# Kernel optimization log

Measured on AMD Instinct MI355X. Metric: run time of the kernel, lower is better.

## Reference

```python
import jax, jax.numpy as jnp
import numpy as np
import math

D = 1024
H = 16
FF = 4096
BS = 4
N = 1024
NEG_INF = -jnp.inf


def layer_norm(x, g, b, eps=1e-5):
    mu = jnp.mean(x, axis=-1, keepdims=True)
    var = jnp.var(x, axis=-1, keepdims=True)
    return (x - mu) * jax.lax.rsqrt(var + eps) * g + b


def mha(x, kv, Wq, Wk, Wv, g, b, causal):
    bs, n, d = x.shape
    n_kv = kv.shape[1]
    hd = d // H
    q = (x @ Wq).reshape(bs, n, H, hd)
    k = (kv @ Wk).reshape(bs, n_kv, H, hd)
    v = (kv @ Wv).reshape(bs, n_kv, H, hd)
    # scores scaled by 1/sqrt(model_dim) as in the original (not head_dim!)
    scores = jnp.einsum('bihd,bjhd->bhij', q, k) / math.sqrt(d)
    if causal:
        i = jnp.arange(n)[:, None]
        j = jnp.arange(n_kv)[None, :]
        scores = jnp.where(j <= i, scores, NEG_INF)
    probs = jax.nn.softmax(scores, axis=-1)
    ctx = jnp.einsum('bhij,bjhd->bihd', probs, v).reshape(bs, n, d)
    return layer_norm(ctx + x, g, b)


def setup_inputs() -> dict:
    key = jax.random.key(0)
    ks = jax.random.split(key, 20)
    s_attn = 1.0 / math.sqrt(D)
    s_ff1 = 1.0 / math.sqrt(D)
    s_ff2 = 1.0 / math.sqrt(FF)
    return {
        'x': jax.random.normal(ks[0], (BS, N, D), jnp.float32),
        'encoder_out': jax.random.normal(ks[1], (BS, N, D), jnp.float32),
        'Wq1': jax.random.normal(ks[2], (D, D), jnp.float32) * s_attn,
        'Wk1': jax.random.normal(ks[3], (D, D), jnp.float32) * s_attn,
        'Wv1': jax.random.normal(ks[4], (D, D), jnp.float32) * s_attn,
        'g1': jnp.ones((D,), jnp.float32), 'b1': jnp.zeros((D,), jnp.float32),
        'Wq2': jax.random.normal(ks[5], (D, D), jnp.float32) * s_attn,
        'Wk2': jax.random.normal(ks[6], (D, D), jnp.float32) * s_attn,
        'Wv2': jax.random.normal(ks[7], (D, D), jnp.float32) * s_attn,
        'g2': jnp.ones((D,), jnp.float32), 'b2': jnp.zeros((D,), jnp.float32),
        'W_ff1': jax.random.normal(ks[8], (D, FF), jnp.float32) * s_ff1,
        'b_ff1': jnp.zeros((FF,), jnp.float32),
        'W_ff2': jax.random.normal(ks[9], (FF, D), jnp.float32) * s_ff2,
        'b_ff2': jnp.zeros((D,), jnp.float32),
        'g3': jnp.ones((D,), jnp.float32), 'b3': jnp.zeros((D,), jnp.float32),
    }


def reference(x, encoder_out, Wq1, Wk1, Wv1, g1, b1, Wq2, Wk2, Wv2, g2, b2,
              W_ff1, b_ff1, W_ff2, b_ff2, g3, b3):
    # masked (causal) self-attention
    x = mha(x, x, Wq1, Wk1, Wv1, g1, b1, causal=True)
    # cross-attention over encoder output
    x = mha(x, encoder_out, Wq2, Wk2, Wv2, g2, b2, causal=False)
    # feedforward with exact GELU, residual, layernorm
    h = jax.nn.gelu(x @ W_ff1 + b_ff1, approximate=False)
    out = h @ W_ff2 + b_ff2
    return layer_norm(out + x, g3, b3)
```

## Files before the change

kernel.cpp:

```cpp
#include <hip/hip_runtime.h>

typedef unsigned short u16;
typedef short bf16x8 __attribute__((ext_vector_type(8)));
typedef float f32x4 __attribute__((ext_vector_type(4)));
typedef unsigned short u16x8 __attribute__((ext_vector_type(8)));
typedef unsigned short u16x4 __attribute__((ext_vector_type(4)));

__device__ __forceinline__ u16 f2bf(float f) {
  unsigned u = __builtin_bit_cast(unsigned, f);
  u += 0x7fffu + ((u >> 16) & 1u);
  return (u16)(u >> 16);
}
__device__ __forceinline__ float bf2f(u16 v) {
  return __builtin_bit_cast(float, (unsigned)v << 16);
}

__device__ __forceinline__ void gload_lds16(const void* g, void* l) {
  __builtin_amdgcn_global_load_lds(
      (const __attribute__((address_space(1))) unsigned int*)g,
      (__attribute__((address_space(3))) unsigned int*)l, 16, 0, 0);
}

__global__ __launch_bounds__(256) void cast2_bf16_kernel(const float* __restrict__ s0,
                                                         u16* __restrict__ d0,
                                                         const float* __restrict__ s1,
                                                         u16* __restrict__ d1) {
  const float* s = blockIdx.y ? s1 : s0;
  u16* d = blockIdx.y ? d1 : d0;
  const size_t i = (size_t)blockIdx.x * 256 + threadIdx.x;
  const float4 a = ((const float4*)s)[2 * i];
  const float4 b = ((const float4*)s)[2 * i + 1];
  u16x8 o;
  o[0] = f2bf(a.x); o[1] = f2bf(a.y); o[2] = f2bf(a.z); o[3] = f2bf(a.w);
  o[4] = f2bf(b.x); o[5] = f2bf(b.y); o[6] = f2bf(b.z); o[7] = f2bf(b.w);
  ((u16x8*)d)[i] = o;
}

__global__ __launch_bounds__(256) void pack_bt3_kernel(const float* __restrict__ W0,
                                                       const float* __restrict__ W1,
                                                       const float* __restrict__ W2,
                                                       u16* __restrict__ Bt,
                                                       int K, int N) {
  const float* W = blockIdx.z == 0 ? W0 : (blockIdx.z == 1 ? W1 : W2);
  u16* dst0 = Bt + (size_t)blockIdx.z * K * N;
  __shared__ u16 sh[64][72];
  const int n0 = blockIdx.x * 64, k0 = blockIdx.y * 64;
  const int t = threadIdx.x;
  {
    const int kloc = t >> 2, nc = (t & 3) * 16;
    const float* src = W + (size_t)(k0 + kloc) * N + n0 + nc;
#pragma unroll
    for (int i = 0; i < 16; ++i) sh[kloc][nc + i] = f2bf(src[i]);
  }
  __syncthreads();
  {
    const int nloc = t >> 2, kc = (t & 3) * 16;
    u16 tmp[16];
#pragma unroll
    for (int i = 0; i < 16; ++i) tmp[i] = sh[kc + i][nloc];
    u16* dst = dst0 + (size_t)(n0 + nloc) * K + k0 + kc;
    *(u16x8*)dst = *(const u16x8*)tmp;
    *(u16x8*)(dst + 8) = *(const u16x8*)(tmp + 8);
  }
}

__global__ __launch_bounds__(256) void pack_bt_kernel(const float* __restrict__ W,
                                                      u16* __restrict__ Bt,
                                                      int K, int N) {
  __shared__ u16 sh[64][72];
  const int n0 = blockIdx.x * 64, k0 = blockIdx.y * 64;
  const int t = threadIdx.x;
  {
    const int kloc = t >> 2, nc = (t & 3) * 16;
    const float* src = W + (size_t)(k0 + kloc) * N + n0 + nc;
#pragma unroll
    for (int i = 0; i < 16; ++i) sh[kloc][nc + i] = f2bf(src[i]);
  }
  __syncthreads();
  {
    const int nloc = t >> 2, kc = (t & 3) * 16;
    u16 tmp[16];
#pragma unroll
    for (int i = 0; i < 16; ++i) tmp[i] = sh[kc + i][nloc];
    u16* dst = Bt + (size_t)(n0 + nloc) * K + k0 + kc;
    *(u16x8*)dst = *(const u16x8*)tmp;
    *(u16x8*)(dst + 8) = *(const u16x8*)(tmp + 8);
  }
}

template <int EPI, int VOUT>
__global__ __launch_bounds__(512, 4) void gemm_bt(const u16* __restrict__ A,
                                                  const u16* __restrict__ Bt,
                                                  void* __restrict__ Cout,
                                                  const float* __restrict__ bias,
                                                  u16* __restrict__ vt, int voff,
                                                  int M, int N, int K, int lda, int ldb) {
  __shared__ u16 lds[2][2][128 * 64];
  const int tid = threadIdx.x;
  const int lane = tid & 63;
  const int wid = tid >> 6;
  const int wr = wid >> 2;
  const int wc = wid & 3;
  const int g = lane >> 4, cc = lane & 15;
  const int nb = N >> 7;
  const int nwg = gridDim.x;
  const int cpx = nwg >> 3;
  const int bid = (blockIdx.x & 7) * cpx + (blockIdx.x >> 3);
  const int bm = bid / nb, bn = bid % nb;
  const size_t arow0 = (size_t)bm << 7;
  const size_t brow0 = (size_t)bn << 7;
  const size_t koff = (size_t)blockIdx.y * K;

  const u16* ap[2];
  const u16* bp[2];
  int ldst[2];
#pragma unroll
  for (int i = 0; i < 2; ++i) {
    const int tt = i * 512 + tid;
    const int row = tt >> 3;
    const int sc8 = ((tt & 7) ^ (row & 7)) * 8;
    ap[i] = A + (arow0 + row) * lda + koff + sc8;
    bp[i] = Bt + (brow0 + row) * ldb + koff + sc8;
    ldst[i] = (i * 512 + wid * 64) * 8;
  }

  int aoff[4], boff[2];
#pragma unroll
  for (int m = 0; m < 4; ++m) {
    const int rowa = wr * 64 + m * 16 + cc;
    aoff[m] = rowa * 128 + ((g ^ (rowa & 7)) << 4);
  }
#pragma unroll
  for (int n = 0; n < 2; ++n) {
    const int rowb = wc * 32 + n * 16 + cc;
    boff[n] = rowb * 128 + ((g ^ (rowb & 7)) << 4);
  }

  f32x4 acc[4][2] = {};
  const int nk = K >> 6;

#pragma unroll
  for (int i = 0; i < 2; ++i) {
    gload_lds16(ap[i], &lds[0][0][ldst[i]]);
    gload_lds16(bp[i], &lds[0][1][ldst[i]]);
    ap[i] += 64;
    bp[i] += 64;
  }
  __syncthreads();

  int cur = 0;
  for (int kk = 0; kk < nk; ++kk) {
    if (kk + 1 < nk) {
#pragma unroll
      for (int i = 0; i < 2; ++i) {
        gload_lds16(ap[i], &lds[cur ^ 1][0][ldst[i]]);
        gload_lds16(bp[i], &lds[cur ^ 1][1][ldst[i]]);
        ap[i] += 64;
        bp[i] += 64;
      }
    }
    const char* Al = (const char*)&lds[cur][0][0];
    const char* Bl = (const char*)&lds[cur][1][0];
    __builtin_amdgcn_s_setprio(1);
#pragma unroll
    for (int ks = 0; ks < 2; ++ks) {
      const int xr = ks << 6;
      bf16x8 af[4], bfr[2];
#pragma unroll
      for (int m = 0; m < 4; ++m)
        af[m] = *(const bf16x8*)(Al + (aoff[m] ^ xr));
#pragma unroll
      for (int n = 0; n < 2; ++n)
        bfr[n] = *(const bf16x8*)(Bl + (boff[n] ^ xr));
#pragma unroll
      for (int m = 0; m < 4; ++m)
#pragma unroll
        for (int n = 0; n < 2; ++n)
          acc[m][n] = __builtin_amdgcn_mfma_f32_16x16x32_bf16(af[m], bfr[n],
                                                              acc[m][n], 0, 0, 0);
    }
    __builtin_amdgcn_s_setprio(0);
    __syncthreads();
    cur ^= 1;
  }

  const size_t pout = (size_t)blockIdx.y * M * N;
#pragma unroll
  for (int m = 0; m < 4; ++m) {
    const size_t gr0 = arow0 + wr * 64 + m * 16 + (g << 2);
#pragma unroll
    for (int n = 0; n < 2; ++n) {
      const size_t gc = brow0 + wc * 32 + n * 16 + cc;
      if (VOUT && (int)gc >= voff) {
        const int col = (int)gc - voff;
        const int hh = col >> 6, dd = col & 63;
        const int bb = (int)(gr0 >> 10), nn = (int)(gr0 & 1023);
        u16x4 ov;
#pragma unroll
        for (int r = 0; r < 4; ++r) ov[r] = f2bf(acc[m][n][r]);
        *(u16x4*)&vt[(((size_t)(bb * 16 + hh) * 64 + dd) << 10) + nn] = ov;
        continue;
      }
      float bv = 0.f;
      if constexpr (EPI == 1) bv = bias[gc];
#pragma unroll
      for (int r = 0; r < 4; ++r) {
        float v = acc[m][n][r] + bv;
        const size_t idx = (gr0 + r) * (size_t)N + gc;
        if constexpr (EPI == 1) {
          const float u2 = 1.5957691216f * (v + 0.044715f * v * v * v);
          const float e = __expf(u2);
          v = v * e / (e + 1.f);
          ((u16*)Cout)[idx] = f2bf(v);
        } else if constexpr (EPI == 0) {
          ((u16*)Cout)[idx] = f2bf(v);
        } else {
          ((float*)Cout)[pout + idx] = v;
        }
      }
    }
  }
}

template <int CAUSAL>
__global__ __launch_bounds__(256, 6) void attn_kernel(const u16* __restrict__ Qb,
                                                      const u16* __restrict__ Kb,
                                                      const u16* __restrict__ Vt,
                                                      u16* __restrict__ Opart,
                                                      float* __restrict__ lpart,
                                                      int qstride, int kstride) {
  const int qt = blockIdx.x;
  const int bh = blockIdx.y;
  const int z = blockIdx.z;
  const int b = bh >> 4, h = bh & 15;
  const int lane = threadIdx.x & 63;
  const int w = threadIdx.x >> 6;
  const int g = lane >> 4, c = lane & 15;
  const int qbase = qt * 64 + w * 16;

  u16* Op = Opart + (size_t)z * 4096 * 1024;
  float* lp = lpart + (size_t)z * 64 * 1024 + (size_t)bh * 1024;

  int kt0 = z * 8, kt1 = z * 8 + 8;
  if (CAUSAL) kt1 = min(kt1, qt + 1);

  if (kt1 <= kt0) {
#pragma unroll
    for (int r = 0; r < 4; ++r) {
      const int qrow = qbase + g * 4 + r;
      u16x4 zz = {0, 0, 0, 0};
      *(u16x4*)&Op[(size_t)(b * 1024 + qrow) * 1024 + h * 64 + c * 4] = zz;
      if (c == 0) lp[qrow] = 0.f;
    }
    return;
  }

  bf16x8 qf0, qf1;
  {
    const int qrow = qbase + c;
    const u16* qp = Qb + (size_t)(b * 1024 + qrow) * qstride + h * 64 + g * 8;
    qf0 = *(const bf16x8*)qp;
    qf1 = *(const bf16x8*)(qp + 32);
  }

  float l_part[4] = {0.f, 0.f, 0.f, 0.f};
  f32x4 oacc[4] = {};

  __shared__ u16 Kl[64 * 64];
  __shared__ u16 Vl[64 * 64];
  __shared__ u16 Pl[4][16 * 72];
  u16* pw = &Pl[w][0];
  const int tid = threadIdx.x;

  for (int kt = kt0; kt < kt1; ++kt) {
    const int kv0 = kt * 64;
    __syncthreads();
#pragma unroll
    for (int i = 0; i < 2; ++i) {
      const int tt = i * 256 + tid;
      const int row = tt >> 3;
      const int sc = (tt & 7) ^ (row & 7);
      gload_lds16(Kb + (size_t)(b * 1024 + kv0 + row) * kstride + h * 64 + sc * 8,
                  &Kl[(size_t)(i * 256 + w * 64) * 8]);
      gload_lds16(Vt + ((size_t)bh * 64 + row) * 1024 + kv0 + sc * 8,
                  &Vl[(size_t)(i * 256 + w * 64) * 8]);
    }
    __syncthreads();

    f32x4 sacc[4] = {};
#pragma unroll
    for (int t = 0; t < 4; ++t) {
      const int row = t * 16 + c;
      const bf16x8 kf0 = *(const bf16x8*)&Kl[row * 64 + (g ^ (row & 7)) * 8];
      const bf16x8 kf1 = *(const bf16x8*)&Kl[row * 64 + ((4 + g) ^ (row & 7)) * 8];
      sacc[t] = __builtin_amdgcn_mfma_f32_16x16x32_bf16(qf0, kf0, sacc[t], 0, 0, 0);
      sacc[t] = __builtin_amdgcn_mfma_f32_16x16x32_bf16(qf1, kf1, sacc[t], 0, 0, 0);
    }
    const int qr0 = qbase + g * 4;
#pragma unroll
    for (int t = 0; t < 4; ++t) {
      const int kvcol = kv0 + t * 16 + c;
      const int col = t * 16 + c;
#pragma unroll
      for (int r = 0; r < 4; ++r) {
        float p = __expf(sacc[t][r] * 0.03125f);
        if (CAUSAL && kvcol > qr0 + r) p = 0.f;
        l_part[r] += p;
        pw[(g * 4 + r) * 72 + col] = f2bf(p);
      }
    }
#pragma unroll
    for (int ks = 0; ks < 2; ++ks) {
      const bf16x8 pa = *(const bf16x8*)&pw[c * 72 + ks * 32 + g * 8];
#pragma unroll
      for (int t2 = 0; t2 < 4; ++t2) {
        const int row = t2 * 16 + c;
        const bf16x8 vb =
            *(const bf16x8*)&Vl[row * 64 + ((ks * 4 + g) ^ (row & 7)) * 8];
        oacc[t2] = __builtin_amdgcn_mfma_f32_16x16x32_bf16(pa, vb, oacc[t2], 0, 0, 0);
      }
    }
  }
#pragma unroll
  for (int xm = 1; xm < 16; xm <<= 1)
#pragma unroll
    for (int r = 0; r < 4; ++r) l_part[r] += __shfl_xor(l_part[r], xm);
  if (c == 0) {
#pragma unroll
    for (int r = 0; r < 4; ++r) lp[qbase + g * 4 + r] = l_part[r];
  }
#pragma unroll
  for (int t2 = 0; t2 < 4; ++t2) {
    const int d = t2 * 16 + c;
#pragma unroll
    for (int r = 0; r < 4; ++r) {
      const int qrow = qbase + g * 4 + r;
      Op[(size_t)(b * 1024 + qrow) * 1024 + h * 64 + d] = f2bf(oacc[t2][r]);
    }
  }
}

template <int MODE, int RES_BF, int OUT_F>
__global__ __launch_bounds__(256) void add_ln_kernel(const void* __restrict__ a,
                                                     const float* __restrict__ lpart,
                                                     const void* __restrict__ res,
                                                     const float* __restrict__ gam,
                                                     const float* __restrict__ bet,
                                                     float* __restrict__ yf,
                                                     u16* __restrict__ ybf,
                                                     const float* __restrict__ bias) {
  const size_t row = blockIdx.x;
  const int t = threadIdx.x;
  float x[4];
  if constexpr (MODE == 1) {
    const u16* Ob = (const u16*)a;
    const u16x4 p0 = ((const u16x4*)(Ob + row * 1024))[t];
    const u16x4 p1 = ((const u16x4*)(Ob + (size_t)4096 * 1024 + row * 1024))[t];
    const int b = (int)(row >> 10), q = (int)(row & 1023);
    const int h = t >> 4;
    const size_t li = (size_t)(b * 16 + h) * 1024 + q;
    const float inv = 1.f / (lpart[li] + lpart[(size_t)64 * 1024 + li]);
#pragma unroll
    for (int i = 0; i < 4; ++i) x[i] = (bf2f(p0[i]) + bf2f(p1[i])) * inv;
  } else {
    const float* af = (const float*)a;
    float4 av = ((const float4*)(af + row * 1024))[t];
    const float4 a2 = ((const float4*)(af + (size_t)4096 * 1024 + row * 1024))[t];
    const float4 bv2 = ((const float4*)bias)[t];
    x[0] = av.x + a2.x + bv2.x; x[1] = av.y + a2.y + bv2.y;
    x[2] = av.z + a2.z + bv2.z; x[3] = av.w + a2.w + bv2.w;
  }
  if constexpr (RES_BF) {
    const u16x4 rv = ((const u16x4*)((const u16*)res + row * 1024))[t];
#pragma unroll
    for (int i = 0; i < 4; ++i) x[i] += bf2f(rv[i]);
  } else {
    const float4 rv = ((const float4*)((const float*)res + row * 1024))[t];
    x[0] += rv.x; x[1] += rv.y; x[2] += rv.z; x[3] += rv.w;
  }
  float s = x[0] + x[1] + x[2] + x[3];
  float q2 = x[0] * x[0] + x[1] * x[1] + x[2] * x[2] + x[3] * x[3];
#pragma unroll
  for (int m = 1; m < 64; m <<= 1) { s += __shfl_xor(s, m); q2 += __shfl_xor(q2, m); }
  __shared__ float ss[4], sq[4];
  const int w = t >> 6;
  if ((t & 63) == 0) { ss[w] = s; sq[w] = q2; }
  __syncthreads();
  s = ss[0] + ss[1] + ss[2] + ss[3];
  q2 = sq[0] + sq[1] + sq[2] + sq[3];
  const float mu = s * (1.f / 1024.f);
  const float var = q2 * (1.f / 1024.f) - mu * mu;
  const float rstd = rsqrtf(var + 1e-5f);
  const float4 gv = ((const float4*)gam)[t];
  const float4 bv = ((const float4*)bet)[t];
  float y[4];
  y[0] = (x[0] - mu) * rstd * gv.x + bv.x;
  y[1] = (x[1] - mu) * rstd * gv.y + bv.y;
  y[2] = (x[2] - mu) * rstd * gv.z + bv.z;
  y[3] = (x[3] - mu) * rstd * gv.w + bv.w;
  if constexpr (OUT_F) {
    float4 o; o.x = y[0]; o.y = y[1]; o.z = y[2]; o.w = y[3];
    ((float4*)(yf + row * 1024))[t] = o;
  } else {
    u16x4 ob;
    ob[0] = f2bf(y[0]); ob[1] = f2bf(y[1]); ob[2] = f2bf(y[2]); ob[3] = f2bf(y[3]);
    ((u16x4*)(ybf + row * 1024))[t] = ob;
  }
}

extern "C" void kernel_launch(void* const* d_in, const int* in_sizes, int n_in,
                              void* d_out, int out_size, void* d_ws, size_t ws_size,
                              hipStream_t stream) {
  const float* x    = (const float*)d_in[0];
  const float* enc  = (const float*)d_in[1];
  const float* Wq1  = (const float*)d_in[2];
  const float* Wk1  = (const float*)d_in[3];
  const float* Wv1  = (const float*)d_in[4];
  const float* g1   = (const float*)d_in[5];
  const float* b1   = (const float*)d_in[6];
  const float* Wq2  = (const float*)d_in[7];
  const float* Wk2  = (const float*)d_in[8];
  const float* Wv2  = (const float*)d_in[9];
  const float* g2   = (const float*)d_in[10];
  const float* b2   = (const float*)d_in[11];
  const float* Wff1 = (const float*)d_in[12];
  const float* bff1 = (const float*)d_in[13];
  const float* Wff2 = (const float*)d_in[14];
  const float* bff2 = (const float*)d_in[15];
  const float* g3   = (const float*)d_in[16];
  const float* b3   = (const float*)d_in[17];
  float* out = (float*)d_out;

  char* ws = (char*)d_ws;
  const size_t MB = 1024ull * 1024ull;
  u16*   bt  = (u16*)(ws + 0 * MB);
  u16*   big = (u16*)(ws + 8 * MB);
  u16*   vt  = (u16*)(ws + 40 * MB);
  float* ctx = (float*)(ws + 48 * MB);
  float* p1f = (float*)(ws + 64 * MB);
  u16*   abf = (u16*)(ws + 96 * MB);
  u16*   ebf = (u16*)(ws + 104 * MB);
  u16*   opart = (u16*)ctx;
  float* lpart = (float*)bt;
  (void)in_sizes; (void)n_in; (void)out_size; (void)ws_size;

  cast2_bf16_kernel<<<dim3(2048, 2), 256, 0, stream>>>(x, abf, enc, ebf);

  pack_bt3_kernel<<<dim3(16, 16, 3), 256, 0, stream>>>(Wq1, Wk1, Wv1, bt, 1024, 1024);
  gemm_bt<0, 1><<<(4096 / 128) * (3072 / 128), 512, 0, stream>>>(
      abf, bt, big, nullptr, vt, 2048, 4096, 3072, 1024, 1024, 1024);
  attn_kernel<1><<<dim3(16, 64, 2), 256, 0, stream>>>(big, big + 1024, vt, opart, lpart,
                                                      3072, 3072);
  add_ln_kernel<1, 0, 0><<<4096, 256, 0, stream>>>(opart, lpart, x, g1, b1,
                                                   nullptr, abf, nullptr);

  pack_bt3_kernel<<<dim3(16, 16, 3), 256, 0, stream>>>(Wq2, Wk2, Wv2, bt, 1024, 1024);
  u16* q2  = big;
  u16* kv2 = big + (size_t)4096 * 1024;
  gemm_bt<0, 0><<<(4096 / 128) * (1024 / 128), 512, 0, stream>>>(
      abf, bt, q2, nullptr, nullptr, 0, 4096, 1024, 1024, 1024, 1024);
  gemm_bt<0, 1><<<(4096 / 128) * (2048 / 128), 512, 0, stream>>>(
      ebf, bt + (size_t)1024 * 1024, kv2, nullptr, vt, 1024, 4096, 2048, 1024, 1024, 1024);
  attn_kernel<0><<<dim3(16, 64, 2), 256, 0, stream>>>(q2, kv2, vt, opart, lpart, 1024, 2048);
  add_ln_kernel<1, 1, 0><<<4096, 256, 0, stream>>>(opart, lpart, abf, g2, b2,
                                                   nullptr, abf, nullptr);

  pack_bt_kernel<<<dim3(64, 16), 256, 0, stream>>>(Wff1, bt, 1024, 4096);
  gemm_bt<1, 0><<<(4096 / 128) * (4096 / 128), 512, 0, stream>>>(
      abf, bt, big, bff1, nullptr, 0, 4096, 4096, 1024, 1024, 1024);
  pack_bt_kernel<<<dim3(16, 64), 256, 0, stream>>>(Wff2, bt, 4096, 1024);
  gemm_bt<3, 0><<<dim3((4096 / 128) * (1024 / 128), 2), 512, 0, stream>>>(
      big, bt, ctx, nullptr, nullptr, 0, 4096, 1024, 2048, 4096, 4096);
  add_ln_kernel<2, 1, 1><<<4096, 256, 0, stream>>>(ctx, nullptr, abf, g3, b3,
                                                   out, nullptr, bff2);
}
```

Measured before the change: 282.4 us.

## Merge weight packing into one launch, unsplit cross-attention, bf16 FF2 partials

All eight weight transposes and bf16 casts now run in a single kernel launch into one packed buffer, replacing four separate pack launches. Cross-attention runs with no KV split and normalizes its output in-kernel, so it no longer writes partial sums and row sums for the layernorm to combine. The split-K FF2 GEMM now writes its partial sums as bf16 instead of fp32, halving that traffic at some cost in precision. The single-pass cross-attention launches half as many blocks, which may reduce GPU occupancy.

```diff
diff --git a/kernel.cpp b/kernel.cpp
--- a/kernel.cpp
+++ b/kernel.cpp
@@ -36,15 +36,34 @@
   ((u16x8*)d)[i] = o;
 }
 
-__global__ __launch_bounds__(256) void pack_bt3_kernel(const float* __restrict__ W0,
-                                                       const float* __restrict__ W1,
-                                                       const float* __restrict__ W2,
-                                                       u16* __restrict__ Bt,
-                                                       int K, int N) {
-  const float* W = blockIdx.z == 0 ? W0 : (blockIdx.z == 1 ? W1 : W2);
-  u16* dst0 = Bt + (size_t)blockIdx.z * K * N;
+__global__ __launch_bounds__(256) void pack_mega_kernel(
+    const float* __restrict__ W0, const float* __restrict__ W1,
+    const float* __restrict__ W2, const float* __restrict__ W3,
+    const float* __restrict__ W4, const float* __restrict__ W5,
+    const float* __restrict__ W6, const float* __restrict__ W7,
+    u16* __restrict__ out) {
+  const int bid = blockIdx.x;
+  const float* W;
+  int K, N, local;
+  size_t dst0;
+  if (bid < 1536) {
+    const int w = bid >> 8;
+    local = bid & 255;
+    K = 1024; N = 1024;
+    W = (w == 0) ? W0 : (w == 1) ? W1 : (w == 2) ? W2 : (w == 3) ? W3 : (w == 4) ? W4 : W5;
+    dst0 = (size_t)w * 1024 * 1024;
+  } else if (bid < 2560) {
+    local = bid - 1536;
+    K = 1024; N = 4096; W = W6;
+    dst0 = (size_t)6 * 1024 * 1024;
+  } else {
+    local = bid - 2560;
+    K = 4096; N = 1024; W = W7;
+    dst0 = (size_t)10 * 1024 * 1024;
+  }
+  const int nx = N >> 6;
+  const int n0 = (local % nx) << 6, k0 = (local / nx) << 6;
   __shared__ u16 sh[64][72];
-  const int n0 = blockIdx.x * 64, k0 = blockIdx.y * 64;
   const int t = threadIdx.x;
   {
     const int kloc = t >> 2, nc = (t & 3) * 16;
@@ -58,31 +77,7 @@
     u16 tmp[16];
 #pragma unroll
     for (int i = 0; i < 16; ++i) tmp[i] = sh[kc + i][nloc];
-    u16* dst = dst0 + (size_t)(n0 + nloc) * K + k0 + kc;
-    *(u16x8*)dst = *(const u16x8*)tmp;
-    *(u16x8*)(dst + 8) = *(const u16x8*)(tmp + 8);
-  }
-}
-
-__global__ __launch_bounds__(256) void pack_bt_kernel(const float* __restrict__ W,
-                                                      u16* __restrict__ Bt,
-                                                      int K, int N) {
-  __shared__ u16 sh[64][72];
-  const int n0 = blockIdx.x * 64, k0 = blockIdx.y * 64;
-  const int t = threadIdx.x;
-  {
-    const int kloc = t >> 2, nc = (t & 3) * 16;
-    const float* src = W + (size_t)(k0 + kloc) * N + n0 + nc;
-#pragma unroll
-    for (int i = 0; i < 16; ++i) sh[kloc][nc + i] = f2bf(src[i]);
-  }
-  __syncthreads();
-  {
-    const int nloc = t >> 2, kc = (t & 3) * 16;
-    u16 tmp[16];
-#pragma unroll
-    for (int i = 0; i < 16; ++i) tmp[i] = sh[kc + i][nloc];
-    u16* dst = Bt + (size_t)(n0 + nloc) * K + k0 + kc;
+    u16* dst = out + dst0 + (size_t)(n0 + nloc) * K + k0 + kc;
     *(u16x8*)dst = *(const u16x8*)tmp;
     *(u16x8*)(dst + 8) = *(const u16x8*)(tmp + 8);
   }
@@ -215,14 +210,14 @@
         } else if constexpr (EPI == 0) {
           ((u16*)Cout)[idx] = f2bf(v);
         } else {
-          ((float*)Cout)[pout + idx] = v;
+          ((u16*)Cout)[pout + idx] = f2bf(v);
         }
       }
     }
   }
 }
 
-template <int CAUSAL>
+template <int CAUSAL, int NZ>
 __global__ __launch_bounds__(256, 6) void attn_kernel(const u16* __restrict__ Qb,
                                                       const u16* __restrict__ Kb,
                                                       const u16* __restrict__ Vt,
@@ -231,7 +226,7 @@
                                                       int qstride, int kstride) {
   const int qt = blockIdx.x;
   const int bh = blockIdx.y;
-  const int z = blockIdx.z;
+  const int z = (NZ == 2) ? blockIdx.z : 0;
   const int b = bh >> 4, h = bh & 15;
   const int lane = threadIdx.x & 63;
   const int w = threadIdx.x >> 6;
@@ -239,12 +234,12 @@
   const int qbase = qt * 64 + w * 16;
 
   u16* Op = Opart + (size_t)z * 4096 * 1024;
-  float* lp = lpart + (size_t)z * 64 * 1024 + (size_t)bh * 1024;
-
-  int kt0 = z * 8, kt1 = z * 8 + 8;
+  float* lp = (NZ == 2) ? lpart + (size_t)z * 64 * 1024 + (size_t)bh * 1024 : nullptr;
+
+  int kt0 = z * (16 / NZ), kt1 = kt0 + 16 / NZ;
   if (CAUSAL) kt1 = min(kt1, qt + 1);
 
-  if (kt1 <= kt0) {
+  if (NZ == 2 && kt1 <= kt0) {
 #pragma unroll
     for (int r = 0; r < 4; ++r) {
       const int qrow = qbase + g * 4 + r;
@@ -325,17 +320,33 @@
   for (int xm = 1; xm < 16; xm <<= 1)
 #pragma unroll
     for (int r = 0; r < 4; ++r) l_part[r] += __shfl_xor(l_part[r], xm);
-  if (c == 0) {
-#pragma unroll
-    for (int r = 0; r < 4; ++r) lp[qbase + g * 4 + r] = l_part[r];
-  }
-#pragma unroll
-  for (int t2 = 0; t2 < 4; ++t2) {
-    const int d = t2 * 16 + c;
-#pragma unroll
-    for (int r = 0; r < 4; ++r) {
-      const int qrow = qbase + g * 4 + r;
-      Op[(size_t)(b * 1024 + qrow) * 1024 + h * 64 + d] = f2bf(oacc[t2][r]);
+
+  if constexpr (NZ == 2) {
+    if (c == 0) {
+#pragma unroll
+      for (int r = 0; r < 4; ++r) lp[qbase + g * 4 + r] = l_part[r];
+    }
+#pragma unroll
+    for (int t2 = 0; t2 < 4; ++t2) {
+      const int d = t2 * 16 + c;
+#pragma unroll
+      for (int r = 0; r < 4; ++r) {
+        const int qrow = qbase + g * 4 + r;
+        Op[(size_t)(b * 1024 + qrow) * 1024 + h * 64 + d] = f2bf(oacc[t2][r]);
+      }
+    }
+  } else {
+    float rl[4];
+#pragma unroll
+    for (int r = 0; r < 4; ++r) rl[r] = 1.f / l_part[r];
+#pragma unroll
+    for (int t2 = 0; t2 < 4; ++t2) {
+      const int d = t2 * 16 + c;
+#pragma unroll
+      for (int r = 0; r < 4; ++r) {
+        const int qrow = qbase + g * 4 + r;
+        Op[(size_t)(b * 1024 + qrow) * 1024 + h * 64 + d] = f2bf(oacc[t2][r] * rl[r]);
+      }
     }
   }
 }
@@ -362,13 +373,20 @@
     const float inv = 1.f / (lpart[li] + lpart[(size_t)64 * 1024 + li]);
 #pragma unroll
     for (int i = 0; i < 4; ++i) x[i] = (bf2f(p0[i]) + bf2f(p1[i])) * inv;
+  } else if constexpr (MODE == 2) {
+    const u16* Ob = (const u16*)a;
+    const u16x4 p0 = ((const u16x4*)(Ob + row * 1024))[t];
+    const u16x4 p1 = ((const u16x4*)(Ob + (size_t)4096 * 1024 + row * 1024))[t];
+    const float4 bv2 = ((const float4*)bias)[t];
+    x[0] = bf2f(p0[0]) + bf2f(p1[0]) + bv2.x;
+    x[1] = bf2f(p0[1]) + bf2f(p1[1]) + bv2.y;
+    x[2] = bf2f(p0[2]) + bf2f(p1[2]) + bv2.z;
+    x[3] = bf2f(p0[3]) + bf2f(p1[3]) + bv2.w;
   } else {
-    const float* af = (const float*)a;
-    float4 av = ((const float4*)(af + row * 1024))[t];
-    const float4 a2 = ((const float4*)(af + (size_t)4096 * 1024 + row * 1024))[t];
-    const float4 bv2 = ((const float4*)bias)[t];
-    x[0] = av.x + a2.x + bv2.x; x[1] = av.y + a2.y + bv2.y;
-    x[2] = av.z + a2.z + bv2.z; x[3] = av.w + a2.w + bv2.w;
+    const u16* Ob = (const u16*)a;
+    const u16x4 p0 = ((const u16x4*)(Ob + row * 1024))[t];
+#pragma unroll
+    for (int i = 0; i < 4; ++i) x[i] = bf2f(p0[i]);
   }
   if constexpr (RES_BF) {
     const u16x4 rv = ((const u16x4*)((const u16*)res + row * 1024))[t];
@@ -433,44 +451,42 @@
 
   char* ws = (char*)d_ws;
   const size_t MB = 1024ull * 1024ull;
-  u16*   bt  = (u16*)(ws + 0 * MB);
-  u16*   big = (u16*)(ws + 8 * MB);
-  u16*   vt  = (u16*)(ws + 40 * MB);
-  float* ctx = (float*)(ws + 48 * MB);
-  float* p1f = (float*)(ws + 64 * MB);
-  u16*   abf = (u16*)(ws + 96 * MB);
-  u16*   ebf = (u16*)(ws + 104 * MB);
-  u16*   opart = (u16*)ctx;
-  float* lpart = (float*)bt;
+  const size_t M1 = 1024ull * 1024ull;
+  u16*   big   = (u16*)(ws + 8 * MB);
+  u16*   vt    = (u16*)(ws + 40 * MB);
+  u16*   opart = (u16*)(ws + 48 * MB);
+  u16*   wpack = (u16*)(ws + 64 * MB);
+  float* lpart = (float*)(ws + 92 * MB);
+  u16*   abf   = (u16*)(ws + 96 * MB);
+  u16*   ebf   = (u16*)(ws + 104 * MB);
   (void)in_sizes; (void)n_in; (void)out_size; (void)ws_size;
 
   cast2_bf16_kernel<<<dim3(2048, 2), 256, 0, stream>>>(x, abf, enc, ebf);
-
-  pack_bt3_kernel<<<dim3(16, 16, 3), 256, 0, stream>>>(Wq1, Wk1, Wv1, bt, 1024, 1024);
+  pack_mega_kernel<<<3584, 256, 0, stream>>>(Wq1, Wk1, Wv1, Wq2, Wk2, Wv2,
+                                             Wff1, Wff2, wpack);
+
   gemm_bt<0, 1><<<(4096 / 128) * (3072 / 128), 512, 0, stream>>>(
-      abf, bt, big, nullptr, vt, 2048, 4096, 3072, 1024, 1024, 1024);
-  attn_kernel<1><<<dim3(16, 64, 2), 256, 0, stream>>>(big, big + 1024, vt, opart, lpart,
-                                                      3072, 3072);
+      abf, wpack, big, nullptr, vt, 2048, 4096, 3072, 1024, 1024, 1024);
+  attn_kernel<1, 2><<<dim3(16, 64, 2), 256, 0, stream>>>(big, big + 1024, vt,
+                                                         opart, lpart, 3072, 3072);
   add_ln_kernel<1, 0, 0><<<4096, 256, 0, stream>>>(opart, lpart, x, g1, b1,
                                                    nullptr, abf, nullptr);
 
-  pack_bt3_kernel<<<dim3(16, 16, 3), 256, 0, stream>>>(Wq2, Wk2, Wv2, bt, 1024, 1024);
   u16* q2  = big;
   u16* kv2 = big + (size_t)4096 * 1024;
   gemm_bt<0, 0><<<(4096 / 128) * (1024 / 128), 512, 0, stream>>>(
-      abf, bt, q2, nullptr, nullptr, 0, 4096, 1024, 1024, 1024, 1024);
+      abf, wpack + 3 * M1, q2, nullptr, nullptr, 0, 4096, 1024, 1024, 1024, 1024);
   gemm_bt<0, 1><<<(4096 / 128) * (2048 / 128), 512, 0, stream>>>(
-      ebf, bt + (size_t)1024 * 1024, kv2, nullptr, vt, 1024, 4096, 2048, 1024, 1024, 1024);
-  attn_kernel<0><<<dim3(16, 64, 2), 256, 0, stream>>>(q2, kv2, vt, opart, lpart, 1024, 2048);
-  add_ln_kernel<1, 1, 0><<<4096, 256, 0, stream>>>(opart, lpart, abf, g2, b2,
+      ebf, wpack + 4 * M1, kv2, nullptr, vt, 1024, 4096, 2048, 1024, 1024, 1024);
+  attn_kernel<0, 1><<<dim3(16, 64, 1), 256, 0, stream>>>(q2, kv2, vt,
+                                                         opart, nullptr, 1024, 2048);
+  add_ln_kernel<3, 1, 0><<<4096, 256, 0, stream>>>(opart, nullptr, abf, g2, b2,
                                                    nullptr, abf, nullptr);
 
-  pack_bt_kernel<<<dim3(64, 16), 256, 0, stream>>>(Wff1, bt, 1024, 4096);
   gemm_bt<1, 0><<<(4096 / 128) * (4096 / 128), 512, 0, stream>>>(
-      abf, bt, big, bff1, nullptr, 0, 4096, 4096, 1024, 1024, 1024);
-  pack_bt_kernel<<<dim3(16, 64), 256, 0, stream>>>(Wff2, bt, 4096, 1024);
+      abf, wpack + 6 * M1, big, bff1, nullptr, 0, 4096, 4096, 1024, 1024, 1024);
   gemm_bt<3, 0><<<dim3((4096 / 128) * (1024 / 128), 2), 512, 0, stream>>>(
-      big, bt, ctx, nullptr, nullptr, 0, 4096, 1024, 2048, 4096, 4096);
-  add_ln_kernel<2, 1, 1><<<4096, 256, 0, stream>>>(ctx, nullptr, abf, g3, b3,
+      big, wpack + 10 * M1, opart, nullptr, nullptr, 0, 4096, 1024, 2048, 4096, 4096);
+  add_ln_kernel<2, 1, 1><<<4096, 256, 0, stream>>>(opart, nullptr, abf, g3, b3,
                                                    out, nullptr, bff2);
 }
```

Result: faster. 269.3 us (-4.6%).
